# Kernel tuning notes

Measured on AMD Instinct MI355X. Metric: run time of the kernel, lower is better.

## Reference

```python
import jax, jax.numpy as jnp
import numpy as np

B, FIN, H, W = 16, 256, 32, 32
NH, FH = 8, 64
CIN = FIN + 2  # fin + 2 coordinate-grid pos channels
COUT = NH * FH


def setup_inputs() -> dict:
    key = jax.random.key(0)
    ks = jax.random.split(key, 9)
    s = 1.0 / np.sqrt(CIN)
    so = 1.0 / np.sqrt(COUT)
    return {
        "x": jax.random.normal(ks[0], (B, FIN, H, W), dtype=jnp.float32),
        "wq": jax.random.uniform(ks[1], (COUT, CIN), jnp.float32, -s, s),
        "bq": jax.random.uniform(ks[2], (COUT,), jnp.float32, -s, s),
        "wk": jax.random.uniform(ks[3], (COUT, CIN), jnp.float32, -s, s),
        "bk": jax.random.uniform(ks[4], (COUT,), jnp.float32, -s, s),
        "wv": jax.random.uniform(ks[5], (COUT, CIN), jnp.float32, -s, s),
        "bv": jax.random.uniform(ks[6], (COUT,), jnp.float32, -s, s),
        "wo": jax.random.uniform(ks[7], (FIN, COUT), jnp.float32, -so, so),
        "bo": jax.random.uniform(ks[8], (FIN,), jnp.float32, -so, so),
    }


def reference(x, wq, bq, wk, bk, wv, bv, wo, bo):
    b, c, h, w = x.shape
    n = h * w
    # PosEncoding: concat one linspace(-1,1) coordinate channel per spatial dim
    gy, gx = jnp.meshgrid(jnp.linspace(-1.0, 1.0, h), jnp.linspace(-1.0, 1.0, w), indexing="ij")
    pos = jnp.broadcast_to(jnp.stack([gy, gx])[None], (b, 2, h, w)).astype(x.dtype)
    t = jnp.concatenate([x, pos], axis=1).reshape(b, c + 2, n)  # [B, C+2, N]
    # 1x1 convs are per-token GEMMs
    q = (jnp.einsum("oc,bcn->bon", wq, t) + bq[:, None]).reshape(b, NH, FH, n)
    k = (jnp.einsum("oc,bcn->bon", wk, t) + bk[:, None]).reshape(b, NH, FH, n)
    v = (jnp.einsum("oc,bcn->bon", wv, t) + bv[:, None]).reshape(b, NH, FH, n)
    temp = FH ** 0.5
    attn = jax.nn.softmax(jnp.einsum("bhdn,bhdm->bhnm", q, k) / temp, axis=-1)
    o = jnp.einsum("bhnm,bhdm->bhdn", attn, v).reshape(b, NH * FH, n)
    o = jnp.einsum("oc,bcn->bon", wo, o) + bo[:, None]
    return x + o.reshape(b, c, h, w)
```

## Files before the change

### kernel.cpp

```cpp
#include <hip/hip_runtime.h>


typedef unsigned short u16;
typedef unsigned int   u32;
typedef __attribute__((ext_vector_type(8))) short  short8;
typedef __attribute__((ext_vector_type(4))) float  float4_;

#define MFMA16(a, b, c) __builtin_amdgcn_mfma_f32_16x16x32_bf16(a, b, c, 0, 0, 0)

__device__ __forceinline__ float bf2f(u16 u) {
    union { u32 i; float f; } v; v.i = ((u32)u) << 16; return v.f;
}
__device__ __forceinline__ u16 f2bf(float f) {
    union { float f; u32 i; } v; v.f = f;
    u32 r = v.i + 0x7FFFu + ((v.i >> 16) & 1u);
    return (u16)(r >> 16);
}
__device__ __forceinline__ u16 f2bf_fast(float f) {
    union { float f; u32 i; } v; v.f = f;
    return (u16)((v.i + 0x8000u) >> 16);
}

__global__ __launch_bounds__(256) void prep(
    const float* __restrict__ wq, const float* __restrict__ wk,
    const float* __restrict__ wv, const float* __restrict__ x,
    u16* __restrict__ wb, u16* __restrict__ xT)
{
    __shared__ float Lt[64][65];
    const int bid = blockIdx.x;
    const int tid = threadIdx.x;
    if (bid < 512) {
        int i = bid * 256 + tid;
        int o = i >> 8, c = i & 255;
        size_t si = (size_t)o * 258 + c;
        wb[i]          = f2bf(wq[si]);
        wb[131072 + i] = f2bf(wk[si]);
        wb[262144 + i] = f2bf(wv[si]);
    } else {
        int r = bid - 512;
        int n0 = (r & 15) * 64, c0 = ((r >> 4) & 3) * 64, b = r >> 6;
#pragma unroll
        for (int p = 0; p < 4; ++p) {
            int c = p * 16 + (tid >> 4);
            int nn = (tid & 15) * 4;
            float4 v = *(const float4*)&x[((size_t)(b * 256) + c0 + c) * 1024 + n0 + nn];
            Lt[c][nn + 0] = v.x; Lt[c][nn + 1] = v.y;
            Lt[c][nn + 2] = v.z; Lt[c][nn + 3] = v.w;
        }
        __syncthreads();
#pragma unroll
        for (int p = 0; p < 4; ++p) {
            int n = p * 16 + (tid >> 4);
            int cc = (tid & 15) * 4;
            ushort4 st;
            st.x = f2bf(Lt[cc + 0][n]); st.y = f2bf(Lt[cc + 1][n]);
            st.z = f2bf(Lt[cc + 2][n]); st.w = f2bf(Lt[cc + 3][n]);
            *(ushort4*)&xT[((size_t)(b << 10) + n0 + n) * 256 + c0 + cc] = st;
        }
    }
}

__global__ __launch_bounds__(256) void qkv_mfma(
    const u16* __restrict__ xT, const u16* __restrict__ wb,
    const float* __restrict__ wq, const float* __restrict__ wk,
    const float* __restrict__ wv,
    const float* __restrict__ bq, const float* __restrict__ bk,
    const float* __restrict__ bv,
    u16* __restrict__ qkvbuf)
{
    __shared__ u16 Wl[128][40];
    __shared__ u16 Tl[128][40];
    const int tid = threadIdx.x;
    const int lane = tid & 63, w = tid >> 6;
    const int quad = lane >> 4, m15 = lane & 15;
    const int n0 = blockIdx.x * 128, mt = blockIdx.y, b = blockIdx.z;
    const int mat = mt >> 2;
    const int m0 = mt * 128;
    const float* worig = (mat == 0) ? wq : ((mat == 1) ? wk : wv);
    const float* bias  = (mat == 0) ? bq : ((mat == 1) ? bk : bv);
    const float oscale = (mat == 1) ? 0.125f : 1.0f;
    u16* outbuf = qkvbuf + (size_t)mat * 8388608;

    float4_ acc[2][8];
#pragma unroll
    for (int s = 0; s < 2; ++s)
#pragma unroll
        for (int t = 0; t < 8; ++t) acc[s][t] = (float4_){0, 0, 0, 0};

    const int row = tid >> 2, col8 = (tid & 3) * 8;

    for (int cc0 = 0; cc0 < 256; cc0 += 32) {
        __syncthreads();
#pragma unroll
        for (int rr = 0; rr < 128; rr += 64) {
            *(short8*)&Wl[row + rr][col8] =
                *(const short8*)(wb + (size_t)(m0 + row + rr) * 256 + cc0 + col8);
            *(short8*)&Tl[row + rr][col8] =
                *(const short8*)(xT + ((size_t)(b << 10) + n0 + row + rr) * 256 + cc0 + col8);
        }
        __syncthreads();
        short8 af[2];
#pragma unroll
        for (int s = 0; s < 2; ++s)
            af[s] = *(const short8*)&Wl[w * 32 + s * 16 + m15][quad * 8];
#pragma unroll
        for (int t = 0; t < 8; ++t) {
            short8 bf = *(const short8*)&Tl[t * 16 + m15][quad * 8];
#pragma unroll
            for (int s = 0; s < 2; ++s)
                acc[s][t] = MFMA16(af[s], bf, acc[s][t]);
        }
    }

#pragma unroll
    for (int s = 0; s < 2; ++s) {
        float wg[4], wx[4], bi[4];
#pragma unroll
        for (int r = 0; r < 4; ++r) {
            int om = (mt & 3) * 128 + w * 32 + s * 16 + quad * 4 + r;
            wg[r] = worig[(size_t)om * 258 + 256];
            wx[r] = worig[(size_t)om * 258 + 257];
            bi[r] = bias[om];
        }
        const int h = (mt & 3) * 2 + ((w * 32 + s * 16) >> 6);
        const int dbase = ((w * 32 + s * 16) & 63) + quad * 4;
#pragma unroll
        for (int t = 0; t < 8; ++t) {
            int n = n0 + t * 16 + m15;
            float gy = -1.0f + 2.0f * (float)(n >> 5) / 31.0f;
            float gx = -1.0f + 2.0f * (float)(n & 31) / 31.0f;
            float v[4];
#pragma unroll
            for (int r = 0; r < 4; ++r)
                v[r] = (acc[s][t][r] + wg[r] * gy + wx[r] * gx + bi[r]) * oscale;
            if (mat != 2) {
                ushort4 st;
                st.x = f2bf(v[0]); st.y = f2bf(v[1]);
                st.z = f2bf(v[2]); st.w = f2bf(v[3]);
                *(ushort4*)&outbuf[((size_t)(b * 8 + h) * 1024 + n) * 64 + dbase] = st;
            } else {
#pragma unroll
                for (int r = 0; r < 4; ++r)
                    outbuf[((size_t)(b * 8 + h) * 64 + dbase + r) * 1024 + n] = f2bf(v[r]);
            }
        }
    }
}

__global__ __launch_bounds__(256) void attn_mfma(
    u16* __restrict__ qbuf, const u16* __restrict__ kbuf,
    const u16* __restrict__ vbuf)
{
    __shared__ u16 Kl[64][72];
    __shared__ u16 Vl[64][72];
    __shared__ u16 Pl[4][32][72];

    const int tid = threadIdx.x;
    const int lane = tid & 63, w = tid >> 6;
    const int quad = lane >> 4, m15 = lane & 15;
    const int q0 = blockIdx.x * 128;
    const int bh = blockIdx.y;
    u16* qb = qbuf + (size_t)bh * 65536;
    const u16* kb = kbuf + (size_t)bh * 65536;
    const u16* vb = vbuf + (size_t)bh * 65536;

    short8 qf[2][2];
#pragma unroll
    for (int s = 0; s < 2; ++s) {
        const u16* qr = qb + (size_t)(q0 + w * 32 + s * 16 + m15) * 64 + quad * 8;
        qf[s][0] = *(const short8*)qr;
        qf[s][1] = *(const short8*)(qr + 32);
    }

    float4_ O[2][4];
    float lp[2][4];
#pragma unroll
    for (int s = 0; s < 2; ++s)
#pragma unroll
        for (int t = 0; t < 4; ++t) { O[s][t] = (float4_){0,0,0,0}; lp[s][t] = 0.0f; }

    const int row = tid >> 3, c8 = (tid & 7) * 8;

    for (int kt0 = 0; kt0 < 1024; kt0 += 64) {
        __syncthreads();
#pragma unroll
        for (int rr = 0; rr < 64; rr += 32) {
            *(short8*)&Kl[row + rr][c8] =
                *(const short8*)(kb + (size_t)(kt0 + row + rr) * 64 + c8);
            *(short8*)&Vl[row + rr][c8] =
                *(const short8*)(vb + (size_t)(row + rr) * 1024 + kt0 + c8);
        }
        __syncthreads();

        float4_ S[2][4];
#pragma unroll
        for (int s = 0; s < 2; ++s)
#pragma unroll
            for (int t = 0; t < 4; ++t) S[s][t] = (float4_){0, 0, 0, 0};
#pragma unroll
        for (int c = 0; c < 2; ++c) {
            short8 bk[4];
#pragma unroll
            for (int t = 0; t < 4; ++t)
                bk[t] = *(const short8*)&Kl[t * 16 + m15][c * 32 + quad * 8];
#pragma unroll
            for (int s = 0; s < 2; ++s)
#pragma unroll
                for (int t = 0; t < 4; ++t)
                    S[s][t] = MFMA16(qf[s][c], bk[t], S[s][t]);
        }

#pragma unroll
        for (int s = 0; s < 2; ++s)
#pragma unroll
            for (int r = 0; r < 4; ++r) {
                float p0 = __expf(S[s][0][r]);
                float p1 = __expf(S[s][1][r]);
                float p2 = __expf(S[s][2][r]);
                float p3 = __expf(S[s][3][r]);
                u16* pr = &Pl[w][s * 16 + quad * 4 + r][m15];
                pr[0]  = f2bf_fast(p0);
                pr[16] = f2bf_fast(p1);
                pr[32] = f2bf_fast(p2);
                pr[48] = f2bf_fast(p3);
                lp[s][r] += (p0 + p1) + (p2 + p3);
            }

#pragma unroll
        for (int c = 0; c < 2; ++c) {
            short8 av[4];
#pragma unroll
            for (int dt = 0; dt < 4; ++dt)
                av[dt] = *(const short8*)&Vl[dt * 16 + m15][c * 32 + quad * 8];
#pragma unroll
            for (int s = 0; s < 2; ++s) {
                short8 bp = *(const short8*)&Pl[w][s * 16 + m15][c * 32 + quad * 8];
#pragma unroll
                for (int dt = 0; dt < 4; ++dt)
                    O[s][dt] = MFMA16(av[dt], bp, O[s][dt]);
            }
        }
    }

#pragma unroll
    for (int s = 0; s < 2; ++s)
#pragma unroll
        for (int r = 0; r < 4; ++r) {
            float v = lp[s][r];
            v += __shfl_xor(v, 1);
            v += __shfl_xor(v, 2);
            v += __shfl_xor(v, 4);
            v += __shfl_xor(v, 8);
            lp[s][r] = v;
        }

#pragma unroll
    for (int s = 0; s < 2; ++s) {
        int src = (m15 >> 2) * 16;
        float a0 = __shfl(lp[s][0], src);
        float a1 = __shfl(lp[s][1], src);
        float a2 = __shfl(lp[s][2], src);
        float a3 = __shfl(lp[s][3], src);
        int rr2 = m15 & 3;
        float lq = (rr2 & 2) ? ((rr2 & 1) ? a3 : a2) : ((rr2 & 1) ? a1 : a0);
        float linv = 1.0f / lq;
        int n = q0 + w * 32 + s * 16 + m15;
#pragma unroll
        for (int dt = 0; dt < 4; ++dt) {
            ushort4 st;
            st.x = f2bf(O[s][dt][0] * linv);
            st.y = f2bf(O[s][dt][1] * linv);
            st.z = f2bf(O[s][dt][2] * linv);
            st.w = f2bf(O[s][dt][3] * linv);
            *(ushort4*)&qb[(size_t)n * 64 + dt * 16 + quad * 4] = st;
        }
    }
}

__global__ __launch_bounds__(256) void proj_mfma(
    const u16* __restrict__ ao, const float* __restrict__ wo,
    const float* __restrict__ bo, const float* __restrict__ x,
    float* __restrict__ out)
{
    __shared__ u16 Wl[64][72];
    __shared__ u16 Tl[64][72];
    const int tid = threadIdx.x;
    const int lane = tid & 63, w = tid >> 6;
    const int quad = lane >> 4, m15 = lane & 15;
    const int n0 = blockIdx.x * 64, f0 = blockIdx.y * 64, b = blockIdx.z;

    float4_ acc[4] = {{0,0,0,0},{0,0,0,0},{0,0,0,0},{0,0,0,0}};
    const int row = tid >> 3, c8 = (tid & 7) * 8;

    for (int cc0 = 0; cc0 < 512; cc0 += 64) {
        __syncthreads();
        const int h = cc0 >> 6;
#pragma unroll
        for (int rr = 0; rr < 64; rr += 32) {
            const float* wsrc = wo + (size_t)(f0 + row + rr) * 512 + cc0 + c8;
            float4 v0 = *(const float4*)wsrc;
            float4 v1 = *(const float4*)(wsrc + 4);
            ushort4 s0, s1;
            s0.x = f2bf(v0.x); s0.y = f2bf(v0.y); s0.z = f2bf(v0.z); s0.w = f2bf(v0.w);
            s1.x = f2bf(v1.x); s1.y = f2bf(v1.y); s1.z = f2bf(v1.z); s1.w = f2bf(v1.w);
            *(ushort4*)&Wl[row + rr][c8]     = s0;
            *(ushort4*)&Wl[row + rr][c8 + 4] = s1;
            *(short8*)&Tl[row + rr][c8] =
                *(const short8*)(ao + ((size_t)((b << 3) + h) * 1024 + n0 + row + rr) * 64 + c8);
        }
        __syncthreads();
#pragma unroll
        for (int c = 0; c < 2; ++c) {
            short8 af = *(const short8*)&Wl[w * 16 + m15][c * 32 + quad * 8];
#pragma unroll
            for (int t = 0; t < 4; ++t) {
                short8 bf = *(const short8*)&Tl[t * 16 + m15][c * 32 + quad * 8];
                acc[t] = MFMA16(af, bf, acc[t]);
            }
        }
    }

    float bi[4];
#pragma unroll
    for (int r = 0; r < 4; ++r) bi[r] = bo[f0 + w * 16 + quad * 4 + r];
#pragma unroll
    for (int t = 0; t < 4; ++t) {
        int n = n0 + t * 16 + m15;
#pragma unroll
        for (int r = 0; r < 4; ++r) {
            int f = f0 + w * 16 + quad * 4 + r;
            size_t idx = ((size_t)(b * 256) + f) * 1024 + n;
            out[idx] = acc[t][r] + bi[r] + x[idx];
        }
    }
}

extern "C" void kernel_launch(void* const* d_in, const int* in_sizes, int n_in,
                              void* d_out, int out_size, void* d_ws, size_t ws_size,
                              hipStream_t stream) {
    const float* x  = (const float*)d_in[0];
    const float* wq = (const float*)d_in[1];
    const float* bq = (const float*)d_in[2];
    const float* wk = (const float*)d_in[3];
    const float* bk = (const float*)d_in[4];
    const float* wv = (const float*)d_in[5];
    const float* bv = (const float*)d_in[6];
    const float* wo = (const float*)d_in[7];
    const float* bo = (const float*)d_in[8];

    u16* qkvbuf = (u16*)d_ws;
    u16* region = qkvbuf + 3 * 8388608;
    u16* xT = region;
    u16* wb = region + 4194304;

    prep<<<1536, 256, 0, stream>>>(wq, wk, wv, x, wb, xT);

    qkv_mfma<<<dim3(8, 12, 16), 256, 0, stream>>>(
        xT, wb, wq, wk, wv, bq, bk, bv, qkvbuf);

    attn_mfma<<<dim3(8, 128), 256, 0, stream>>>(
        qkvbuf, qkvbuf + 8388608, qkvbuf + 16777216);

    proj_mfma<<<dim3(16, 4, 16), 256, 0, stream>>>(qkvbuf, wo, bo, x, (float*)d_out);
}
```

Baseline: 202.4 us.

## Pre-convert wo to bf16, enlarge proj tiles, reorder attention grid

The prep kernel now also converts the output projection weight wo to bf16, so proj_mfma no longer converts fp32 weights on every tile load. proj_mfma moves from 64x64 to 128x128 output tiles, with each wave computing 2x8 MFMA fragments to raise data reuse from LDS. The attention grid is transposed so consecutive blocks walk different batch-heads instead of the query tiles of one head. In exchange the proj grid shrinks to 256 blocks, which may underfill the GPU, and register and LDS use per block go up.

New measurement: 210.6 us. 4.0% more time.

```diff
diff --git a/kernel.cpp b/kernel.cpp
--- a/kernel.cpp
+++ b/kernel.cpp
@@ -23,8 +23,9 @@
 
 __global__ __launch_bounds__(256) void prep(
     const float* __restrict__ wq, const float* __restrict__ wk,
-    const float* __restrict__ wv, const float* __restrict__ x,
-    u16* __restrict__ wb, u16* __restrict__ xT)
+    const float* __restrict__ wv, const float* __restrict__ wo,
+    const float* __restrict__ x,
+    u16* __restrict__ wb, u16* __restrict__ xT, u16* __restrict__ wbo)
 {
     __shared__ float Lt[64][65];
     const int bid = blockIdx.x;
@@ -36,7 +37,7 @@
         wb[i]          = f2bf(wq[si]);
         wb[131072 + i] = f2bf(wk[si]);
         wb[262144 + i] = f2bf(wv[si]);
-    } else {
+    } else if (bid < 1536) {
         int r = bid - 512;
         int n0 = (r & 15) * 64, c0 = ((r >> 4) & 3) * 64, b = r >> 6;
 #pragma unroll
@@ -57,6 +58,9 @@
             st.z = f2bf(Lt[cc + 2][n]); st.w = f2bf(Lt[cc + 3][n]);
             *(ushort4*)&xT[((size_t)(b << 10) + n0 + n) * 256 + c0 + cc] = st;
         }
+    } else {
+        int i = (bid - 1536) * 256 + tid;
+        wbo[i] = f2bf(wo[i]);
     }
 }
 
@@ -158,8 +162,8 @@
     const int tid = threadIdx.x;
     const int lane = tid & 63, w = tid >> 6;
     const int quad = lane >> 4, m15 = lane & 15;
-    const int q0 = blockIdx.x * 128;
-    const int bh = blockIdx.y;
+    const int q0 = blockIdx.y * 128;
+    const int bh = blockIdx.x;
     u16* qb = qbuf + (size_t)bh * 65536;
     const u16* kb = kbuf + (size_t)bh * 65536;
     const u16* vb = vbuf + (size_t)bh * 65536;
@@ -278,59 +282,66 @@
 }
 
 __global__ __launch_bounds__(256) void proj_mfma(
-    const u16* __restrict__ ao, const float* __restrict__ wo,
+    const u16* __restrict__ ao, const u16* __restrict__ wob,
     const float* __restrict__ bo, const float* __restrict__ x,
     float* __restrict__ out)
 {
-    __shared__ u16 Wl[64][72];
-    __shared__ u16 Tl[64][72];
+    __shared__ u16 Wl[128][72];
+    __shared__ u16 Tl[128][72];
     const int tid = threadIdx.x;
     const int lane = tid & 63, w = tid >> 6;
     const int quad = lane >> 4, m15 = lane & 15;
-    const int n0 = blockIdx.x * 64, f0 = blockIdx.y * 64, b = blockIdx.z;
-
-    float4_ acc[4] = {{0,0,0,0},{0,0,0,0},{0,0,0,0},{0,0,0,0}};
-    const int row = tid >> 3, c8 = (tid & 7) * 8;
+    const int n0 = blockIdx.x * 128, f0 = blockIdx.y * 128, b = blockIdx.z;
+
+    float4_ acc[2][8];
+#pragma unroll
+    for (int s = 0; s < 2; ++s)
+#pragma unroll
+        for (int t = 0; t < 8; ++t) acc[s][t] = (float4_){0, 0, 0, 0};
+
+    const int row2 = tid >> 1, colh = (tid & 1) * 32;
 
     for (int cc0 = 0; cc0 < 512; cc0 += 64) {
         __syncthreads();
         const int h = cc0 >> 6;
 #pragma unroll
-        for (int rr = 0; rr < 64; rr += 32) {
-            const float* wsrc = wo + (size_t)(f0 + row + rr) * 512 + cc0 + c8;
-            float4 v0 = *(const float4*)wsrc;
-            float4 v1 = *(const float4*)(wsrc + 4);
-            ushort4 s0, s1;
-            s0.x = f2bf(v0.x); s0.y = f2bf(v0.y); s0.z = f2bf(v0.z); s0.w = f2bf(v0.w);
-            s1.x = f2bf(v1.x); s1.y = f2bf(v1.y); s1.z = f2bf(v1.z); s1.w = f2bf(v1.w);
-            *(ushort4*)&Wl[row + rr][c8]     = s0;
-            *(ushort4*)&Wl[row + rr][c8 + 4] = s1;
-            *(short8*)&Tl[row + rr][c8] =
-                *(const short8*)(ao + ((size_t)((b << 3) + h) * 1024 + n0 + row + rr) * 64 + c8);
+        for (int j = 0; j < 4; ++j) {
+            *(short8*)&Wl[row2][colh + j * 8] =
+                *(const short8*)(wob + (size_t)(f0 + row2) * 512 + cc0 + colh + j * 8);
+            *(short8*)&Tl[row2][colh + j * 8] =
+                *(const short8*)(ao + ((size_t)((b << 3) + h) * 1024 + n0 + row2) * 64 + colh + j * 8);
         }
         __syncthreads();
 #pragma unroll
         for (int c = 0; c < 2; ++c) {
-            short8 af = *(const short8*)&Wl[w * 16 + m15][c * 32 + quad * 8];
-#pragma unroll
-            for (int t = 0; t < 4; ++t) {
+            short8 af[2];
+#pragma unroll
+            for (int s = 0; s < 2; ++s)
+                af[s] = *(const short8*)&Wl[w * 32 + s * 16 + m15][c * 32 + quad * 8];
+#pragma unroll
+            for (int t = 0; t < 8; ++t) {
                 short8 bf = *(const short8*)&Tl[t * 16 + m15][c * 32 + quad * 8];
-                acc[t] = MFMA16(af, bf, acc[t]);
-            }
-        }
-    }
-
-    float bi[4];
-#pragma unroll
-    for (int r = 0; r < 4; ++r) bi[r] = bo[f0 + w * 16 + quad * 4 + r];
-#pragma unroll
-    for (int t = 0; t < 4; ++t) {
-        int n = n0 + t * 16 + m15;
-#pragma unroll
-        for (int r = 0; r < 4; ++r) {
-            int f = f0 + w * 16 + quad * 4 + r;
-            size_t idx = ((size_t)(b * 256) + f) * 1024 + n;
-            out[idx] = acc[t][r] + bi[r] + x[idx];
+#pragma unroll
+                for (int s = 0; s < 2; ++s)
+                    acc[s][t] = MFMA16(af[s], bf, acc[s][t]);
+            }
+        }
+    }
+
+#pragma unroll
+    for (int s = 0; s < 2; ++s) {
+        float bi[4];
+#pragma unroll
+        for (int r = 0; r < 4; ++r) bi[r] = bo[f0 + w * 32 + s * 16 + quad * 4 + r];
+#pragma unroll
+        for (int t = 0; t < 8; ++t) {
+            int n = n0 + t * 16 + m15;
+#pragma unroll
+            for (int r = 0; r < 4; ++r) {
+                int f = f0 + w * 32 + s * 16 + quad * 4 + r;
+                size_t idx = ((size_t)(b * 256) + f) * 1024 + n;
+                out[idx] = acc[s][t][r] + bi[r] + x[idx];
+            }
         }
     }
 }
@@ -350,16 +361,18 @@
 
     u16* qkvbuf = (u16*)d_ws;
     u16* region = qkvbuf + 3 * 8388608;
-    u16* xT = region;
-    u16* wb = region + 4194304;
-
-    prep<<<1536, 256, 0, stream>>>(wq, wk, wv, x, wb, xT);
+    u16* xT  = region;
+    u16* wb  = region + 4194304;
+    u16* wbo = wb + 393216;
+
+    prep<<<2048, 256, 0, stream>>>(wq, wk, wv, wo, x, wb, xT, wbo);
 
     qkv_mfma<<<dim3(8, 12, 16), 256, 0, stream>>>(
         xT, wb, wq, wk, wv, bq, bk, bv, qkvbuf);
 
-    attn_mfma<<<dim3(8, 128), 256, 0, stream>>>(
+    attn_mfma<<<dim3(128, 8), 256, 0, stream>>>(
         qkvbuf, qkvbuf + 8388608, qkvbuf + 16777216);
 
-    proj_mfma<<<dim3(16, 4, 16), 256, 0, stream>>>(qkvbuf, wo, bo, x, (float*)d_out);
-}
+    proj_mfma<<<dim3(8, 2, 16), 256, 0, stream>>>(
+        qkvbuf, wbo, bo, x, (float*)d_out);
+}
```
